# Performance work log

Measured on AMD Instinct MI355X. Metric: run time of the kernel, lower is better.

## Reference

```python
import jax, jax.numpy as jnp
import numpy as np
from jax import lax

HID = 768          # hidden_dim / embedding_dim
IN = 64            # input_dim = max_seq_length // num_heads
SEQ = 512          # max_seq_length
GROUPS = IN        # conv groups
BLUR_K = 5
BLUR_SIGMA = 1.0


def _gauss1d(k, sigma):
    half = (k - 1) * 0.5
    x = np.linspace(-half, half, k)
    pdf = np.exp(-0.5 * (x / sigma) ** 2)
    return pdf / pdf.sum()


def setup_inputs() -> dict:
    key = jax.random.key(0)
    ks = jax.random.split(key, 8)
    s = 0.02
    return {
        "inputs": jax.random.normal(ks[0], (16, SEQ, HID), jnp.float32),
        # Conv1d(768, 768, k=3, groups=64): weight [out_ch, in_ch/groups, k]
        "conv_w": jax.random.normal(ks[1], (HID, HID // GROUPS, 3), jnp.float32) * s,
        "conv_b": jnp.zeros((HID,), jnp.float32),
        "ln_g": jnp.ones((IN,), jnp.float32),
        "ln_b": jnp.zeros((IN,), jnp.float32),
        # function_info: Linear(64, 64), torch weight convention [out, in]
        "fi_w": jax.random.normal(ks[2], (IN, IN), jnp.float32) * s,
        "fi_b": jnp.zeros((IN,), jnp.float32),
        # block_info: Linear(64, 1)
        "bi_w": jax.random.normal(ks[3], (1, IN), jnp.float32) * s,
        "bi_b": jnp.zeros((1,), jnp.float32),
    }


def _forward(inputs, conv_w, conv_b, ln_g, ln_b, fi_w, fi_b, bi_w, bi_b):
    x = inputs.reshape(-1, HID, IN)  # [Bn, 768, 64] (raw row-major view, as torch .view)
    q = k = v = m = x

    # q: grouped Conv1d + residual, GELU, LayerNorm over last dim (64)
    qc = lax.conv_general_dilated(
        q, conv_w, window_strides=(1,), padding=[(1, 1)],
        feature_group_count=GROUPS, dimension_numbers=("NCH", "OIH", "NCH"))
    qc = qc + conv_b[None, :, None]
    q = jax.nn.gelu(qc + q, approximate=False)
    mu = jnp.mean(q, axis=-1, keepdims=True)
    var = jnp.mean(jnp.square(q - mu), axis=-1, keepdims=True)
    q = (q - mu) * lax.rsqrt(var + 1e-5) * ln_g + ln_b

    # v: Linear(64,64) + GELU
    v = jax.nn.gelu(v @ fi_w.T + fi_b, approximate=False)

    # k: dropout (eval -> identity), softmax over dim=-2 (channel axis), GELU
    k = jax.nn.gelu(jax.nn.softmax(k, axis=-2), approximate=False)

    # m: GaussianBlur(5, sigma fixed 1.0) over (H=768, W=64) with reflect pad, then Linear(64,1)
    g = _gauss1d(BLUR_K, BLUR_SIGMA)
    kern = jnp.asarray(np.outer(g, g), m.dtype)[None, None]  # [1,1,5,5]
    p = BLUR_K // 2
    mp = jnp.pad(m[:, None], ((0, 0), (0, 0), (p, p), (p, p)), mode="reflect")
    m = lax.conv_general_dilated(
        mp, kern, (1, 1), "VALID", dimension_numbers=("NCHW", "OIHW", "NCHW"))[:, 0]
    m = m @ bi_w.T + bi_b                        # [Bn, 768, 1]
    mask = jnp.broadcast_to(m, (m.shape[0], HID, HID))  # expand to [Bn,768,768]

    # SDPA: scale = 1/sqrt(E) with E = q.shape[-1] = 64; additive float mask
    scores = jnp.einsum("bce,bde->bcd", q, k) * (1.0 / np.sqrt(IN)) + mask
    attn = jax.nn.softmax(scores, axis=-1)
    out = jnp.einsum("bcd,bde->bce", attn, v)    # [Bn, 768, 64]
    return out.reshape(-1, SEQ, HID)


def reference(inputs, conv_w, conv_b, ln_g, ln_b, fi_w, fi_b, bi_w, bi_b):
    return _forward(inputs, conv_w, conv_b, ln_g, ln_b, fi_w, fi_b, bi_w, bi_b)
```

## Files before the change

kernel.cpp:

```cpp
#include <hip/hip_runtime.h>
#include <hip/hip_bf16.h>
#include <math.h>

#define NB 128
#define NC 768
#define NE 64
#define IPG 12

typedef __hip_bfloat16 bf16;
typedef __bf16 bf16v8 __attribute__((ext_vector_type(8)));
typedef __bf16 bf16v4 __attribute__((ext_vector_type(4)));
typedef __bf16 bf16v2 __attribute__((ext_vector_type(2)));
typedef float f32x4 __attribute__((ext_vector_type(4)));
typedef unsigned int u32;
typedef u32 u32x4 __attribute__((ext_vector_type(4)));

__device__ __forceinline__ float gelu_exact(float x) {
    float ax = fabsf(x);
    float t = __builtin_amdgcn_rcpf(fmaf(0.2316419f, ax, 1.0f));
    float poly = t * fmaf(t, fmaf(t, fmaf(t, fmaf(t, 1.330274429f,
                  -1.821255978f), 1.781477937f), -0.356563782f), 0.319381530f);
    float pdf = 0.3989422804f * __expf(-0.5f * ax * ax);
    float c = fmaf(-pdf, poly, 1.0f);
    float cdf = (x >= 0.f) ? c : 1.0f - c;
    return x * cdf;
}

#define MFMA16(a, b, c) __builtin_amdgcn_mfma_f32_16x16x32_bf16(a, b, c, 0, 0, 0)

__device__ __forceinline__ void gload_lds16(const void* g, void* l) {
    __builtin_amdgcn_global_load_lds(
        (const __attribute__((address_space(1))) void*)g,
        (__attribute__((address_space(3))) void*)l, 16, 0, 0);
}

__global__ __launch_bounds__(256) void k_conv(
    const float* __restrict__ x, const float* __restrict__ cw,
    const float* __restrict__ cb, const float* __restrict__ lg,
    const float* __restrict__ lb, bf16* __restrict__ qo,
    float* __restrict__ sp)
{
    int b = blockIdx.x >> 4;
    int chunk = blockIdx.x & 15;
    int w = threadIdx.x >> 6;
    int g = __builtin_amdgcn_readfirstlane(chunk * 4 + w);
    int h = threadIdx.x & 63;
    const float* xb = x + ((size_t)b * NC + g * IPG) * NE;

    float xi[IPG], xm[IPG], xp[IPG];
    #pragma unroll
    for (int i = 0; i < IPG; ++i) {
        xi[i] = xb[i * NE + h];
        float up = __shfl_up(xi[i], 1);
        float dn = __shfl_down(xi[i], 1);
        xm[i] = h ? up : 0.f;
        xp[i] = (h < 63) ? dn : 0.f;
    }

    float es = 0.f;
    #pragma unroll
    for (int i = 0; i < IPG; ++i) es += __expf(xi[i]);
    __shared__ float red[4][64];
    red[w][h] = es;
    __syncthreads();
    if (w == 0) {
        float s = red[0][h] + red[1][h] + red[2][h] + red[3][h];
        sp[(size_t)(b * 16 + chunk) * 64 + h] = s;
    }

    float gam = lg[h], bet = lb[h];
    const float* wg = cw + (size_t)g * IPG * 36;

    for (int o = 0; o < IPG; ++o) {
        const float* wo = wg + o * 36;
        float acc = cb[g * IPG + o];
        #pragma unroll
        for (int i = 0; i < IPG; ++i)
            acc = fmaf(xm[i], wo[i*3], fmaf(xi[i], wo[i*3+1], fmaf(xp[i], wo[i*3+2], acc)));
        float gl = gelu_exact(acc + xi[o]);
        float s1 = gl, s2 = gl * gl;
        #pragma unroll
        for (int off = 32; off; off >>= 1) {
            s1 += __shfl_xor(s1, off);
            s2 += __shfl_xor(s2, off);
        }
        float mu  = s1 * (1.f / 64.f);
        float var = s2 * (1.f / 64.f) - mu * mu;
        float qn = (gl - mu) * rsqrtf(var + 1e-5f) * gam + bet;
        qo[((size_t)b * NC + g * IPG + o) * NE + h] = __float2bfloat16(qn * 0.125f);
    }
}

__global__ __launch_bounds__(256) void k_vk(
    const float* __restrict__ x, const float* __restrict__ fw,
    const float* __restrict__ fb, const float* __restrict__ sp,
    bf16* __restrict__ ko, bf16* __restrict__ vt2)
{
    int chunk = blockIdx.x, b = blockIdx.y;
    int tid = threadIdx.x, w = tid >> 6, l = tid & 63;
    int lr = l & 15, lc = (l >> 4) * 8;
    int rowb = chunk * 64 + w * 16;
    const float* xb = x + (size_t)b * NC * NE;

    __shared__ float sts[64];
    if (tid < 64) {
        float s = 0.f;
        #pragma unroll
        for (int p = 0; p < 16; ++p) s += sp[(size_t)(b * 16 + p) * 64 + tid];
        sts[tid] = 1.f / s;
    }

    bf16v8 bfr[4][2];
    float fbias[4];
    #pragma unroll
    for (int nt = 0; nt < 4; ++nt) {
        #pragma unroll
        for (int kt = 0; kt < 2; ++kt) {
            const float* p = fw + (nt*16 + lr) * 64 + kt*32 + lc;
            bf16v8 t;
            #pragma unroll
            for (int j = 0; j < 8; ++j) t[j] = (__bf16)p[j];
            bfr[nt][kt] = t;
        }
        fbias[nt] = fb[nt*16 + lr];
    }
    __syncthreads();

    float isA[8], isB[8];
    #pragma unroll
    for (int j = 0; j < 8; ++j) { isA[j] = sts[lc + j]; isB[j] = sts[32 + lc + j]; }

    const float* pa = xb + (size_t)(rowb + lr) * NE;
    float xa[8], xc[8];
    #pragma unroll
    for (int j = 0; j < 8; ++j) xa[j] = pa[lc + j];
    #pragma unroll
    for (int j = 0; j < 8; ++j) xc[j] = pa[32 + lc + j];

    bf16v8 a0, a1;
    #pragma unroll
    for (int j = 0; j < 8; ++j) a0[j] = (__bf16)xa[j];
    #pragma unroll
    for (int j = 0; j < 8; ++j) a1[j] = (__bf16)xc[j];

    bf16v8 kv0, kv1;
    #pragma unroll
    for (int j = 0; j < 8; ++j) kv0[j] = (__bf16)gelu_exact(__expf(xa[j]) * isA[j]);
    #pragma unroll
    for (int j = 0; j < 8; ++j) kv1[j] = (__bf16)gelu_exact(__expf(xc[j]) * isB[j]);
    bf16* kp = ko + ((size_t)b * NC + rowb + lr) * NE + lc;
    *(bf16v8*)kp = kv0;
    *(bf16v8*)(kp + 32) = kv1;

    int c0 = rowb + (l >> 4) * 4;
    int ktile = c0 >> 5, kc = c0 & 31;
    #pragma unroll
    for (int nt = 0; nt < 4; ++nt) {
        f32x4 acc = {fbias[nt], fbias[nt], fbias[nt], fbias[nt]};
        acc = MFMA16(a0, bfr[nt][0], acc);
        acc = MFMA16(a1, bfr[nt][1], acc);
        bf16v4 pk;
        #pragma unroll
        for (int r = 0; r < 4; ++r) pk[r] = (__bf16)gelu_exact(acc[r]);
        *(bf16v4*)&vt2[(((size_t)b * 24 + ktile) * 64 + nt*16 + lr) * 32 + kc] = pk;
    }
}

__device__ __forceinline__ bf16v8 softmax_exch(f32x4 s0, f32x4 s1, float& rsum,
                                               int srcA, int srcB, int hq) {
    float p0 = __expf(s0[0]), p1 = __expf(s0[1]), p2 = __expf(s0[2]), p3 = __expf(s0[3]);
    float p4 = __expf(s1[0]), p5 = __expf(s1[1]), p6 = __expf(s1[2]), p7 = __expf(s1[3]);
    rsum += ((p0 + p1) + (p2 + p3)) + ((p4 + p5) + (p6 + p7));
    bf16v2 t0; t0[0] = (__bf16)p0; t0[1] = (__bf16)p1;
    bf16v2 t1; t1[0] = (__bf16)p2; t1[1] = (__bf16)p3;
    bf16v2 t2; t2[0] = (__bf16)p4; t2[1] = (__bf16)p5;
    bf16v2 t3; t3[0] = (__bf16)p6; t3[1] = (__bf16)p7;
    u32 w0 = __builtin_bit_cast(u32, t0), w1 = __builtin_bit_cast(u32, t1);
    u32 w2 = __builtin_bit_cast(u32, t2), w3 = __builtin_bit_cast(u32, t3);
    u32 c0A = (u32)__shfl((int)w0, srcA), c1A = (u32)__shfl((int)w1, srcA);
    u32 c2A = (u32)__shfl((int)w2, srcA), c3A = (u32)__shfl((int)w3, srcA);
    u32 c0B = (u32)__shfl((int)w0, srcB), c1B = (u32)__shfl((int)w1, srcB);
    u32 c2B = (u32)__shfl((int)w2, srcB), c3B = (u32)__shfl((int)w3, srcB);
    u32x4 pau = { hq ? c2A : c0A, hq ? c3A : c1A,
                  hq ? c2B : c0B, hq ? c3B : c1B };
    return __builtin_bit_cast(bf16v8, pau);
}

__global__ __launch_bounds__(256, 3) void k_attn(const bf16* __restrict__ qb,
                                                 const bf16* __restrict__ kb,
                                                 const bf16* __restrict__ vt2,
                                                 float* __restrict__ out) {
    __shared__ __align__(16) __bf16 ldsK[2][4096];
    __shared__ __align__(16) __bf16 ldsV[2][4096];

    int bid = blockIdx.x;
    int swz = (bid & 7) * 96 + (bid >> 3);
    int b = swz / 6, qt = swz - b * 6;
    int w = threadIdx.x >> 6, l = threadIdx.x & 63;
    int q0 = qt * 128 + w * 32;
    int lr = l & 15, hi = l >> 4;
    int hq = hi >> 1;
    int srcA = lr + ((hi & 1) << 5);
    int srcB = srcA + 16;

    int krow_ = w * 8 + (l >> 3);
    int kc16_ = (l & 7) ^ (l >> 3);
    const char* kgbase = (const char*)(kb + (size_t)b * NC * NE)
                       + krow_ * 128 + kc16_ * 16;
    int ve_   = w * 16 + (l >> 2);
    int vc16_ = (l & 3) ^ ((l >> 3) & 3);
    const char* vgbase = (const char*)vt2 + (size_t)b * 24 * 4096
                       + ve_ * 64 + vc16_ * 16;

    int krd0 = lr * 64 + ((hi ^ (lr & 7)) << 3);
    int krd1 = lr * 64 + (((4 + hi) ^ (lr & 7)) << 3);
    int vsel = (lr >> 1) & 3;
    int vrd  = lr * 32 + ((hi ^ vsel) << 3);

    const bf16* qp = qb + ((size_t)b * NC + q0 + lr) * NE + hi * 8;
    bf16v8 qf00 = *(const bf16v8*)qp;
    bf16v8 qf01 = *(const bf16v8*)(qp + 32);
    bf16v8 qf10 = *(const bf16v8*)(qp + 16 * NE);
    bf16v8 qf11 = *(const bf16v8*)(qp + 16 * NE + 32);

    f32x4 o00 = {0,0,0,0}, o01 = {0,0,0,0}, o02 = {0,0,0,0}, o03 = {0,0,0,0};
    f32x4 o10 = {0,0,0,0}, o11 = {0,0,0,0}, o12 = {0,0,0,0}, o13 = {0,0,0,0};
    float rsum0 = 0.f, rsum1 = 0.f;

    gload_lds16(kgbase,        &ldsK[0][w * 512]);
    gload_lds16(kgbase + 4096, &ldsK[0][2048 + w * 512]);
    gload_lds16(vgbase,        &ldsV[0][w * 512]);
    gload_lds16(vgbase + 4096, &ldsV[0][2048 + w * 512]);
    __syncthreads();

    int cur = 0;
    for (int ph = 0; ph < 12; ++ph) {
        if (ph < 11) {
            const char* kg = kgbase + (size_t)(2 * ph + 2) * 4096;
            gload_lds16(kg,        &ldsK[cur ^ 1][w * 512]);
            gload_lds16(kg + 4096, &ldsK[cur ^ 1][2048 + w * 512]);
            const char* vg = vgbase + (size_t)(2 * ph + 2) * 4096;
            gload_lds16(vg,        &ldsV[cur ^ 1][w * 512]);
            gload_lds16(vg + 4096, &ldsV[cur ^ 1][2048 + w * 512]);
        }

        #pragma unroll
        for (int sub = 0; sub < 2; ++sub) {
            const __bf16* Kc = &ldsK[cur][sub * 2048];
            const __bf16* Vc = &ldsV[cur][sub * 2048];
            bf16v8 ka0 = *(const bf16v8*)&Kc[krd0];
            bf16v8 ka1 = *(const bf16v8*)&Kc[krd1];
            bf16v8 ka2 = *(const bf16v8*)&Kc[krd0 + 1024];
            bf16v8 ka3 = *(const bf16v8*)&Kc[krd1 + 1024];
            bf16v8 v0  = *(const bf16v8*)&Vc[vrd];
            bf16v8 v1  = *(const bf16v8*)&Vc[vrd + 512];
            bf16v8 v2  = *(const bf16v8*)&Vc[vrd + 1024];
            bf16v8 v3  = *(const bf16v8*)&Vc[vrd + 1536];

            __builtin_amdgcn_s_setprio(1);
            f32x4 s00 = {0,0,0,0}, s01 = {0,0,0,0};
            s00 = MFMA16(ka0, qf00, s00);
            s00 = MFMA16(ka1, qf01, s00);
            s01 = MFMA16(ka2, qf00, s01);
            s01 = MFMA16(ka3, qf01, s01);
            f32x4 s10 = {0,0,0,0}, s11 = {0,0,0,0};
            s10 = MFMA16(ka0, qf10, s10);
            s10 = MFMA16(ka1, qf11, s10);
            s11 = MFMA16(ka2, qf10, s11);
            s11 = MFMA16(ka3, qf11, s11);
            __builtin_amdgcn_s_setprio(0);

            bf16v8 pa0 = softmax_exch(s00, s01, rsum0, srcA, srcB, hq);
            bf16v8 pa1 = softmax_exch(s10, s11, rsum1, srcA, srcB, hq);

            __builtin_amdgcn_s_setprio(1);
            o00 = MFMA16(pa0, v0, o00);
            o01 = MFMA16(pa0, v1, o01);
            o02 = MFMA16(pa0, v2, o02);
            o03 = MFMA16(pa0, v3, o03);
            o10 = MFMA16(pa1, v0, o10);
            o11 = MFMA16(pa1, v1, o11);
            o12 = MFMA16(pa1, v2, o12);
            o13 = MFMA16(pa1, v3, o13);
            __builtin_amdgcn_s_setprio(0);
        }

        __syncthreads();
        cur ^= 1;
    }

    rsum0 += __shfl_xor(rsum0, 16);
    rsum0 += __shfl_xor(rsum0, 32);
    rsum1 += __shfl_xor(rsum1, 16);
    rsum1 += __shfl_xor(rsum1, 32);
    float inv0 = 1.f / rsum0, inv1 = 1.f / rsum1;

    int qrow0 = q0 + hi * 4;
    #pragma unroll
    for (int r = 0; r < 4; ++r) {
        float iq = __shfl(inv0, hi * 4 + r);
        float* op = out + ((size_t)b * NC + qrow0 + r) * NE + lr;
        op[0]  = o00[r] * iq;
        op[16] = o01[r] * iq;
        op[32] = o02[r] * iq;
        op[48] = o03[r] * iq;
    }
    int qrow1 = q0 + 16 + hi * 4;
    #pragma unroll
    for (int r = 0; r < 4; ++r) {
        float iq = __shfl(inv1, hi * 4 + r);
        float* op = out + ((size_t)b * NC + qrow1 + r) * NE + lr;
        op[0]  = o10[r] * iq;
        op[16] = o11[r] * iq;
        op[32] = o12[r] * iq;
        op[48] = o13[r] * iq;
    }
}

extern "C" void kernel_launch(void* const* d_in, const int* in_sizes, int n_in,
                              void* d_out, int out_size, void* d_ws, size_t ws_size,
                              hipStream_t stream) {
    (void)in_sizes; (void)n_in; (void)out_size; (void)ws_size;
    const float* x      = (const float*)d_in[0];
    const float* conv_w = (const float*)d_in[1];
    const float* conv_b = (const float*)d_in[2];
    const float* ln_g   = (const float*)d_in[3];
    const float* ln_b   = (const float*)d_in[4];
    const float* fi_w   = (const float*)d_in[5];
    const float* fi_b   = (const float*)d_in[6];

    bf16* qbuf = (bf16*)d_ws;
    bf16* kbuf = qbuf + (size_t)NB * NC * NE;
    bf16* vt2  = kbuf + (size_t)NB * NC * NE;
    float* stats = (float*)(vt2 + (size_t)NB * NC * NE);
    float* out = (float*)d_out;

    k_conv<<<dim3(NB * 16), 256, 0, stream>>>(x, conv_w, conv_b, ln_g, ln_b,
                                              qbuf, stats);
    k_vk<<<dim3(12, NB), 256, 0, stream>>>(x, fi_w, fi_b, stats, kbuf, vt2);
    k_attn<<<dim3(768), 256, 0, stream>>>(qbuf, kbuf, vt2, out);
}
```

Before: 78.27 us.

## Move V projection into conv kernel and slim K-building kernel

The Linear+GELU V projection moves out of the k/v kernel into the conv kernel, now called k_prod. That kernel uses 8 chunks per batch, each processing two conv groups per wave plus 96 rows of V tiles. The second kernel now only builds the softmax-over-channels K tensor from the column exp-sum stats. This rebalances work between the two pre-attention kernels so the dependent second kernel is lighter. In exchange it uses fewer, heavier blocks (1024 vs 2048) and uneven wave usage in the V loop, since only 6 tiles are split across 4 waves.

```diff
diff --git a/kernel.cpp b/kernel.cpp
--- a/kernel.cpp
+++ b/kernel.cpp
@@ -34,81 +34,64 @@
         (__attribute__((address_space(3))) void*)l, 16, 0, 0);
 }
 
-__global__ __launch_bounds__(256) void k_conv(
+__global__ __launch_bounds__(256) void k_prod(
     const float* __restrict__ x, const float* __restrict__ cw,
     const float* __restrict__ cb, const float* __restrict__ lg,
-    const float* __restrict__ lb, bf16* __restrict__ qo,
-    float* __restrict__ sp)
+    const float* __restrict__ lb, const float* __restrict__ fw,
+    const float* __restrict__ fb, bf16* __restrict__ qo,
+    float* __restrict__ sp, bf16* __restrict__ vt2)
 {
-    int b = blockIdx.x >> 4;
-    int chunk = blockIdx.x & 15;
-    int w = threadIdx.x >> 6;
-    int g = __builtin_amdgcn_readfirstlane(chunk * 4 + w);
-    int h = threadIdx.x & 63;
-    const float* xb = x + ((size_t)b * NC + g * IPG) * NE;
-
-    float xi[IPG], xm[IPG], xp[IPG];
-    #pragma unroll
-    for (int i = 0; i < IPG; ++i) {
-        xi[i] = xb[i * NE + h];
-        float up = __shfl_up(xi[i], 1);
-        float dn = __shfl_down(xi[i], 1);
-        xm[i] = h ? up : 0.f;
-        xp[i] = (h < 63) ? dn : 0.f;
-    }
+    int chunk = blockIdx.x;
+    int b = blockIdx.y;
+    int w = threadIdx.x >> 6, h = threadIdx.x & 63;
+    const float* xb = x + (size_t)b * NC * NE;
+    float gam = lg[h], bet = lb[h];
 
     float es = 0.f;
-    #pragma unroll
-    for (int i = 0; i < IPG; ++i) es += __expf(xi[i]);
+    for (int gi = 0; gi < 2; ++gi) {
+        int g = __builtin_amdgcn_readfirstlane(chunk * 8 + gi * 4 + w);
+        const float* xg = xb + (size_t)g * IPG * NE;
+
+        float xi[IPG], xm[IPG], xp[IPG];
+        #pragma unroll
+        for (int i = 0; i < IPG; ++i) {
+            xi[i] = xg[i * NE + h];
+            float up = __shfl_up(xi[i], 1);
+            float dn = __shfl_down(xi[i], 1);
+            xm[i] = h ? up : 0.f;
+            xp[i] = (h < 63) ? dn : 0.f;
+            es += __expf(xi[i]);
+        }
+        const float* wg = cw + (size_t)g * IPG * 36;
+        for (int o = 0; o < IPG; ++o) {
+            const float* wo = wg + o * 36;
+            float acc = cb[g * IPG + o];
+            #pragma unroll
+            for (int i = 0; i < IPG; ++i)
+                acc = fmaf(xm[i], wo[i*3], fmaf(xi[i], wo[i*3+1], fmaf(xp[i], wo[i*3+2], acc)));
+            float gl = gelu_exact(acc + xi[o]);
+            float s1 = gl, s2 = gl * gl;
+            #pragma unroll
+            for (int off = 32; off; off >>= 1) {
+                s1 += __shfl_xor(s1, off);
+                s2 += __shfl_xor(s2, off);
+            }
+            float mu  = s1 * (1.f / 64.f);
+            float var = s2 * (1.f / 64.f) - mu * mu;
+            float qn = (gl - mu) * rsqrtf(var + 1e-5f) * gam + bet;
+            qo[((size_t)b * NC + g * IPG + o) * NE + h] = __float2bfloat16(qn * 0.125f);
+        }
+    }
+
     __shared__ float red[4][64];
     red[w][h] = es;
     __syncthreads();
-    if (w == 0) {
-        float s = red[0][h] + red[1][h] + red[2][h] + red[3][h];
-        sp[(size_t)(b * 16 + chunk) * 64 + h] = s;
-    }
-
-    float gam = lg[h], bet = lb[h];
-    const float* wg = cw + (size_t)g * IPG * 36;
-
-    for (int o = 0; o < IPG; ++o) {
-        const float* wo = wg + o * 36;
-        float acc = cb[g * IPG + o];
-        #pragma unroll
-        for (int i = 0; i < IPG; ++i)
-            acc = fmaf(xm[i], wo[i*3], fmaf(xi[i], wo[i*3+1], fmaf(xp[i], wo[i*3+2], acc)));
-        float gl = gelu_exact(acc + xi[o]);
-        float s1 = gl, s2 = gl * gl;
-        #pragma unroll
-        for (int off = 32; off; off >>= 1) {
-            s1 += __shfl_xor(s1, off);
-            s2 += __shfl_xor(s2, off);
-        }
-        float mu  = s1 * (1.f / 64.f);
-        float var = s2 * (1.f / 64.f) - mu * mu;
-        float qn = (gl - mu) * rsqrtf(var + 1e-5f) * gam + bet;
-        qo[((size_t)b * NC + g * IPG + o) * NE + h] = __float2bfloat16(qn * 0.125f);
-    }
-}
-
-__global__ __launch_bounds__(256) void k_vk(
-    const float* __restrict__ x, const float* __restrict__ fw,
-    const float* __restrict__ fb, const float* __restrict__ sp,
-    bf16* __restrict__ ko, bf16* __restrict__ vt2)
-{
-    int chunk = blockIdx.x, b = blockIdx.y;
-    int tid = threadIdx.x, w = tid >> 6, l = tid & 63;
+    if (w == 0)
+        sp[(size_t)(b * 8 + chunk) * 64 + h] =
+            red[0][h] + red[1][h] + red[2][h] + red[3][h];
+
+    int l = threadIdx.x & 63;
     int lr = l & 15, lc = (l >> 4) * 8;
-    int rowb = chunk * 64 + w * 16;
-    const float* xb = x + (size_t)b * NC * NE;
-
-    __shared__ float sts[64];
-    if (tid < 64) {
-        float s = 0.f;
-        #pragma unroll
-        for (int p = 0; p < 16; ++p) s += sp[(size_t)(b * 16 + p) * 64 + tid];
-        sts[tid] = 1.f / s;
-    }
 
     bf16v8 bfr[4][2];
     float fbias[4];
@@ -124,46 +107,62 @@
         }
         fbias[nt] = fb[nt*16 + lr];
     }
+
+    for (int t = w; t < 6; t += 4) {
+        int trow = chunk * 96 + t * 16;
+        const float* pa = xb + (size_t)(trow + lr) * NE;
+        bf16v8 a0, a1;
+        #pragma unroll
+        for (int j = 0; j < 8; ++j) a0[j] = (__bf16)pa[lc + j];
+        #pragma unroll
+        for (int j = 0; j < 8; ++j) a1[j] = (__bf16)pa[32 + lc + j];
+
+        int c0 = trow + (l >> 4) * 4;
+        int ktile = c0 >> 5, kc = c0 & 31;
+        #pragma unroll
+        for (int nt = 0; nt < 4; ++nt) {
+            f32x4 acc = {fbias[nt], fbias[nt], fbias[nt], fbias[nt]};
+            acc = MFMA16(a0, bfr[nt][0], acc);
+            acc = MFMA16(a1, bfr[nt][1], acc);
+            bf16v4 pk;
+            #pragma unroll
+            for (int r = 0; r < 4; ++r) pk[r] = (__bf16)gelu_exact(acc[r]);
+            *(bf16v4*)&vt2[(((size_t)b * 24 + ktile) * 64 + nt*16 + lr) * 32 + kc] = pk;
+        }
+    }
+}
+
+__global__ __launch_bounds__(256) void k_kbuild(
+    const float* __restrict__ x, const float* __restrict__ sp,
+    bf16* __restrict__ ko)
+{
+    int chunk = blockIdx.x, b = blockIdx.y;
+    int tid = threadIdx.x, w = tid >> 6, l = tid & 63;
+    int lr = l & 15, lc = (l >> 4) * 8;
+    int rowb = chunk * 64 + w * 16;
+
+    __shared__ float sts[64];
+    if (tid < 64) {
+        float s = 0.f;
+        #pragma unroll
+        for (int p = 0; p < 8; ++p) s += sp[(size_t)(b * 8 + p) * 64 + tid];
+        sts[tid] = 1.f / s;
+    }
     __syncthreads();
 
     float isA[8], isB[8];
     #pragma unroll
     for (int j = 0; j < 8; ++j) { isA[j] = sts[lc + j]; isB[j] = sts[32 + lc + j]; }
 
-    const float* pa = xb + (size_t)(rowb + lr) * NE;
-    float xa[8], xc[8];
-    #pragma unroll
-    for (int j = 0; j < 8; ++j) xa[j] = pa[lc + j];
-    #pragma unroll
-    for (int j = 0; j < 8; ++j) xc[j] = pa[32 + lc + j];
-
-    bf16v8 a0, a1;
-    #pragma unroll
-    for (int j = 0; j < 8; ++j) a0[j] = (__bf16)xa[j];
-    #pragma unroll
-    for (int j = 0; j < 8; ++j) a1[j] = (__bf16)xc[j];
-
+    const float* pa = x + ((size_t)b * NC + rowb + lr) * NE;
     bf16v8 kv0, kv1;
     #pragma unroll
-    for (int j = 0; j < 8; ++j) kv0[j] = (__bf16)gelu_exact(__expf(xa[j]) * isA[j]);
-    #pragma unroll
-    for (int j = 0; j < 8; ++j) kv1[j] = (__bf16)gelu_exact(__expf(xc[j]) * isB[j]);
+    for (int j = 0; j < 8; ++j) kv0[j] = (__bf16)gelu_exact(__expf(pa[lc + j]) * isA[j]);
+    #pragma unroll
+    for (int j = 0; j < 8; ++j) kv1[j] = (__bf16)gelu_exact(__expf(pa[32 + lc + j]) * isB[j]);
     bf16* kp = ko + ((size_t)b * NC + rowb + lr) * NE + lc;
     *(bf16v8*)kp = kv0;
     *(bf16v8*)(kp + 32) = kv1;
-
-    int c0 = rowb + (l >> 4) * 4;
-    int ktile = c0 >> 5, kc = c0 & 31;
-    #pragma unroll
-    for (int nt = 0; nt < 4; ++nt) {
-        f32x4 acc = {fbias[nt], fbias[nt], fbias[nt], fbias[nt]};
-        acc = MFMA16(a0, bfr[nt][0], acc);
-        acc = MFMA16(a1, bfr[nt][1], acc);
-        bf16v4 pk;
-        #pragma unroll
-        for (int r = 0; r < 4; ++r) pk[r] = (__bf16)gelu_exact(acc[r]);
-        *(bf16v4*)&vt2[(((size_t)b * 24 + ktile) * 64 + nt*16 + lr) * 32 + kc] = pk;
-    }
 }
 
 __device__ __forceinline__ bf16v8 softmax_exch(f32x4 s0, f32x4 s1, float& rsum,
@@ -335,8 +334,8 @@
     float* stats = (float*)(vt2 + (size_t)NB * NC * NE);
     float* out = (float*)d_out;
 
-    k_conv<<<dim3(NB * 16), 256, 0, stream>>>(x, conv_w, conv_b, ln_g, ln_b,
-                                              qbuf, stats);
-    k_vk<<<dim3(12, NB), 256, 0, stream>>>(x, fi_w, fi_b, stats, kbuf, vt2);
+    k_prod<<<dim3(8, NB), 256, 0, stream>>>(x, conv_w, conv_b, ln_g, ln_b,
+                                            fi_w, fi_b, qbuf, stats, vt2);
+    k_kbuild<<<dim3(12, NB), 256, 0, stream>>>(x, stats, kbuf);
     k_attn<<<dim3(768), 256, 0, stream>>>(qbuf, kbuf, vt2, out);
 }
```

After: 79.64 us. No clear change (+1.8%).
